# Kernel tuning notes

Hardware: AMD Instinct MI355X
Metric: run time of the kernel (lower is better)

## Reference

```python
import jax, jax.numpy as jnp
import numpy as np

B, S = 32768, 512  # rays, max bright spots (= 2*max_samples)


def setup_inputs() -> dict:
    key = jax.random.key(0)
    k1, k2, k3, k4, k5 = jax.random.split(key, 5)
    V = jax.random.normal(k1, (B, 3), dtype=jnp.float32)
    N = jax.random.normal(k2, (B, 3), dtype=jnp.float32)
    N = N / jnp.linalg.norm(N, axis=-1, keepdims=True)
    spots = jax.random.normal(k3, (S, 3), dtype=jnp.float32)
    spots = spots / jnp.linalg.norm(spots, axis=-1, keepdims=True)
    # prefix masks: num_ele[i] <= num_ray[i] <= S (matches kernel's start_ind-j indexing)
    num_ray = jax.random.randint(k4, (B,), S // 2, S + 1)
    num_ele = jax.random.randint(k5, (B,), 0, S // 2)
    j = jnp.arange(S)
    ray_mask = j[None, :] < num_ray[:, None]
    bright_mask = j[None, :] < num_ele[:, None]
    std = jnp.float32(0.05)  # pix_size
    return {"V": V, "N": N, "spots": spots, "ray_mask": ray_mask,
            "bright_mask": bright_mask, "std": std}


def reference(V, N, spots, ray_mask, bright_mask, std):
    Bn, Sn = bright_mask.shape
    # wp.randf(seed): uniform in [0,1), one per written component -> (B,S,3)
    u = jax.random.uniform(jax.random.key(42), (Bn, Sn, 3), dtype=spots.dtype)
    num_ele = bright_mask.sum(axis=1)            # n per row
    num_ray = ray_mask.sum(axis=1)               # start_ind = num_ray - 1
    j = jnp.arange(Sn)
    active = j[None, :] < num_ele[:, None]       # j in range(n)
    jit = spots[None, :, :] + std * u            # jittered light dirs (B,S,3)
    LdotN = jnp.einsum('bsd,bd->bs', jit, N)
    cond = active & (LdotN > 0.0)                # rejection test
    t = num_ray[:, None] - 1 - j[None, :]        # reversed write index
    t_safe = jnp.where(cond & (t >= 0) & (t < Sn), t, Sn)  # Sn -> dropped
    b_idx = jnp.arange(Bn)[:, None]
    Ls = jnp.zeros((Bn, Sn, 3), spots.dtype).at[b_idx, t_safe].set(jit, mode='drop')
    bmask = jnp.zeros((Bn, Sn), jnp.int32).at[b_idx, t_safe].set(1, mode='drop')
    return Ls, bmask.astype(bool)
```

## Files before the change

### kernel.cpp

```cpp
#include <hip/hip_runtime.h>


#define TF_ROUND(x0, x1, r) { x0 += x1; x1 = ((x1 << (r)) | (x1 >> (32 - (r)))); x1 ^= x0; }

__device__ __forceinline__ unsigned tf2x32_seed42_xor(unsigned x0, unsigned x1) {
  const unsigned k0 = 0u, k1 = 42u;
  const unsigned k2 = 0x1BD11BDAu ^ k0 ^ k1;
  x0 += k0; x1 += k1;
  TF_ROUND(x0,x1,13) TF_ROUND(x0,x1,15) TF_ROUND(x0,x1,26) TF_ROUND(x0,x1,6)
  x0 += k1; x1 += k2 + 1u;
  TF_ROUND(x0,x1,17) TF_ROUND(x0,x1,29) TF_ROUND(x0,x1,16) TF_ROUND(x0,x1,24)
  x0 += k2; x1 += k0 + 2u;
  TF_ROUND(x0,x1,13) TF_ROUND(x0,x1,15) TF_ROUND(x0,x1,26) TF_ROUND(x0,x1,6)
  x0 += k0; x1 += k1 + 3u;
  TF_ROUND(x0,x1,17) TF_ROUND(x0,x1,29) TF_ROUND(x0,x1,16) TF_ROUND(x0,x1,24)
  x0 += k1; x1 += k2 + 4u;
  TF_ROUND(x0,x1,13) TF_ROUND(x0,x1,15) TF_ROUND(x0,x1,26) TF_ROUND(x0,x1,6)
  x0 += k2; x1 += k0 + 5u;
  return x0 ^ x1;
}

typedef float f4v __attribute__((ext_vector_type(4)));

__device__ __forceinline__ int detect_mode(const unsigned char* m) {
  const unsigned char d0 = m[0], d1 = m[1], d4 = m[4];
  return (d0 == 0) ? 3 : ((d1 != 0) ? 0 : ((d4 != 0) ? 1 : 2));
}

__global__ __launch_bounds__(64, 8) void bis_row(
    const float* __restrict__ Nrm, const float* __restrict__ spots,
    const unsigned char* __restrict__ rmask, const unsigned char* __restrict__ emask,
    const float* __restrict__ stdp, float* __restrict__ Ls, float* __restrict__ bm)
{
  const int b = blockIdx.x;
  const int l = threadIdx.x;
  __shared__ f4v s_jit[256];

  const int mode = detect_mode(rmask);
  const unsigned base = (unsigned)b * 512u + (unsigned)(l << 3);

  int rcnt = 0, ecnt = 0;
  if (mode == 0) {
    const uint2 rv = *(const uint2*)(rmask + base);
    const uint2 ev = *(const uint2*)(emask + base);
    rcnt = __popc(rv.x & 0x01010101u) + __popc(rv.y & 0x01010101u);
    ecnt = __popc(ev.x & 0x01010101u) + __popc(ev.y & 0x01010101u);
  } else if (mode == 1) {
    const int* rp = (const int*)rmask + base; const int* ep = (const int*)emask + base;
    const int4 r0 = *(const int4*)rp, r1 = *(const int4*)(rp + 4);
    const int4 e0 = *(const int4*)ep, e1 = *(const int4*)(ep + 4);
    rcnt = (r0.x!=0)+(r0.y!=0)+(r0.z!=0)+(r0.w!=0)+(r1.x!=0)+(r1.y!=0)+(r1.z!=0)+(r1.w!=0);
    ecnt = (e0.x!=0)+(e0.y!=0)+(e0.z!=0)+(e0.w!=0)+(e1.x!=0)+(e1.y!=0)+(e1.z!=0)+(e1.w!=0);
  } else if (mode == 3) {
    const float* rp = (const float*)rmask + base; const float* ep = (const float*)emask + base;
    const float4 r0 = *(const float4*)rp, r1 = *(const float4*)(rp + 4);
    const float4 e0 = *(const float4*)ep, e1 = *(const float4*)(ep + 4);
    rcnt = (r0.x!=0.f)+(r0.y!=0.f)+(r0.z!=0.f)+(r0.w!=0.f)+(r1.x!=0.f)+(r1.y!=0.f)+(r1.z!=0.f)+(r1.w!=0.f);
    ecnt = (e0.x!=0.f)+(e0.y!=0.f)+(e0.z!=0.f)+(e0.w!=0.f)+(e1.x!=0.f)+(e1.y!=0.f)+(e1.z!=0.f)+(e1.w!=0.f);
  } else {
    const long long* rp = (const long long*)rmask; const long long* ep = (const long long*)emask;
    #pragma unroll
    for (int c = 0; c < 8; ++c) { rcnt += rp[base+c] != 0; ecnt += ep[base+c] != 0; }
  }
  unsigned pack = (unsigned)rcnt | ((unsigned)ecnt << 16);
  #pragma unroll
  for (int off = 1; off < 64; off <<= 1) pack += __shfl_xor(pack, off, 64);
  const int num_ray = (int)(pack & 0xFFFFu);
  const int num_ele = (int)(pack >> 16);

  if (num_ele > 0) {
    const float stdv = stdp[0];
    const float n0 = Nrm[b*3+0], n1 = Nrm[b*3+1], n2 = Nrm[b*3+2];
    for (int j = l; j < num_ele; j += 64) {
      const unsigned f = ((unsigned)b * 512u + (unsigned)j) * 3u;
      const float u0 = __uint_as_float((tf2x32_seed42_xor(0u, f + 0u) >> 9) | 0x3F800000u) - 1.0f;
      const float u1 = __uint_as_float((tf2x32_seed42_xor(0u, f + 1u) >> 9) | 0x3F800000u) - 1.0f;
      const float u2 = __uint_as_float((tf2x32_seed42_xor(0u, f + 2u) >> 9) | 0x3F800000u) - 1.0f;
      const float j0 = __fadd_rn(spots[j*3+0], __fmul_rn(stdv, u0));
      const float j1 = __fadd_rn(spots[j*3+1], __fmul_rn(stdv, u1));
      const float j2 = __fadd_rn(spots[j*3+2], __fmul_rn(stdv, u2));
      const float d  = __fadd_rn(__fadd_rn(__fmul_rn(j0,n0), __fmul_rn(j1,n1)),
                                 __fmul_rn(j2,n2));
      const bool acc = (d > 0.0f);
      f4v e; e.x = acc ? j0 : 0.f; e.y = acc ? j1 : 0.f; e.z = acc ? j2 : 0.f;
      e.w = acc ? 1.f : 0.f;
      s_jit[j] = e;
    }
  }
  __syncthreads();

  const int lo = num_ray - num_ele;
  const int hi = num_ray;
  const float* jrow = (const float*)s_jit;

  f4v* lsrow = (f4v*)(Ls + (size_t)b * 1536u);
  #pragma unroll
  for (int i = 0; i < 6; ++i) {
    const int g = i * 64 + l;
    const unsigned ff0 = (unsigned)(g << 2);
    const int s0 = (int)((ff0 * 43691u) >> 17);
    const int s1 = (int)(((ff0 + 3u) * 43691u) >> 17);
    f4v o = {0.f, 0.f, 0.f, 0.f};
    if (s1 >= lo && s0 < hi) {
      #pragma unroll
      for (int k = 0; k < 4; ++k) {
        const unsigned ff = ff0 + (unsigned)k;
        const unsigned s  = (ff * 43691u) >> 17;
        const unsigned comp = ff - 3u * s;
        const int jj = num_ray - 1 - (int)s;
        if (jj >= 0 && jj < num_ele) o[k] = jrow[(unsigned)jj * 4u + comp];
      }
    }
    lsrow[g] = o;
  }

  f4v* bmrow = (f4v*)(bm + (size_t)b * 512u);
  #pragma unroll
  for (int i = 0; i < 2; ++i) {
    const int g = i * 64 + l;
    const int sb = g << 2;
    f4v o = {0.f, 0.f, 0.f, 0.f};
    if (sb + 3 >= lo && sb < hi) {
      #pragma unroll
      for (int k = 0; k < 4; ++k) {
        const int jj = num_ray - 1 - (sb + k);
        if (jj >= 0 && jj < num_ele) o[k] = jrow[(unsigned)jj * 4u + 3u];
      }
    }
    bmrow[g] = o;
  }
}

struct F3 { float x, y, z; };

__global__ __launch_bounds__(512) void bis_kernel_s(
    const float* __restrict__ Nrm, const float* __restrict__ spots,
    const unsigned char* __restrict__ rmask, const unsigned char* __restrict__ emask,
    const float* __restrict__ stdp, float* __restrict__ Ls, float* __restrict__ bm,
    int S)
{
  const long long b = blockIdx.x;
  const int t = threadIdx.x;
  const int mode = detect_mode(rmask);

  const long long e = b * (long long)S + t;
  int rnz, enz;
  if (mode == 0)      { rnz = rmask[e] != 0;                     enz = emask[e] != 0; }
  else if (mode == 1) { rnz = ((const int*)rmask)[e] != 0;       enz = ((const int*)emask)[e] != 0; }
  else if (mode == 2) { rnz = ((const long long*)rmask)[e] != 0; enz = ((const long long*)emask)[e] != 0; }
  else                { rnz = ((const float*)rmask)[e] != 0.0f;  enz = ((const float*)emask)[e] != 0.0f; }

  __shared__ int s_nr[16], s_ne[16];
  const unsigned long long br = __ballot(rnz);
  const unsigned long long be = __ballot(enz);
  const int w = t >> 6;
  if ((t & 63) == 0) { s_nr[w] = __popcll(br); s_ne[w] = __popcll(be); }
  __syncthreads();
  const int nw = blockDim.x >> 6;
  int num_ray = 0, num_ele = 0;
  for (int i = 0; i < nw; ++i) { num_ray += s_nr[i]; num_ele += s_ne[i]; }

  const int j = num_ray - 1 - t;
  float o0 = 0.f, o1 = 0.f, o2 = 0.f, m = 0.f;
  if (j >= 0 && j < num_ele) {
    const float stdv = stdp[0];
    const float n0 = Nrm[b*3+0], n1 = Nrm[b*3+1], n2 = Nrm[b*3+2];
    const unsigned f = (unsigned)((b * (long long)S + j) * 3LL);
    const float u0 = __uint_as_float((tf2x32_seed42_xor(0u, f + 0u) >> 9) | 0x3F800000u) - 1.0f;
    const float u1 = __uint_as_float((tf2x32_seed42_xor(0u, f + 1u) >> 9) | 0x3F800000u) - 1.0f;
    const float u2 = __uint_as_float((tf2x32_seed42_xor(0u, f + 2u) >> 9) | 0x3F800000u) - 1.0f;
    const float j0 = __fadd_rn(spots[j*3+0], __fmul_rn(stdv, u0));
    const float j1 = __fadd_rn(spots[j*3+1], __fmul_rn(stdv, u1));
    const float j2 = __fadd_rn(spots[j*3+2], __fmul_rn(stdv, u2));
    const float d  = __fadd_rn(__fadd_rn(__fmul_rn(j0,n0), __fmul_rn(j1,n1)), __fmul_rn(j2,n2));
    if (d > 0.0f) { o0 = j0; o1 = j1; o2 = j2; m = 1.0f; }
  }

  const long long oidx = b * (long long)S + t;
  F3 v; v.x = o0; v.y = o1; v.z = o2;
  reinterpret_cast<F3*>(Ls)[oidx] = v;
  bm[oidx] = m;
}

extern "C" void kernel_launch(void* const* d_in, const int* in_sizes, int n_in,
                              void* d_out, int out_size, void* d_ws, size_t ws_size,
                              hipStream_t stream) {
  const float* Nrm = (const float*)d_in[1];
  const float* spots = (const float*)d_in[2];
  const unsigned char* rmask = (const unsigned char*)d_in[3];
  const unsigned char* emask = (const unsigned char*)d_in[4];
  const float* stdp = (const float*)d_in[5];

  const int B = in_sizes[0] / 3;
  const int S = in_sizes[2] / 3;

  float* out = (float*)d_out;
  float* Ls = out;
  float* bm = out + (long long)B * S * 3;

  if (S == 512) {
    dim3 grid((unsigned)B), block(64);
    hipLaunchKernelGGL(bis_row, grid, block, 0, stream,
                       Nrm, spots, rmask, emask, stdp, Ls, bm);
  } else {
    dim3 grid((unsigned)B), block((unsigned)S);
    hipLaunchKernelGGL(bis_kernel_s, grid, block, 0, stream,
                       Nrm, spots, rmask, emask, stdp, Ls, bm, S);
  }
}
```

Baseline: 82.88 us.

## Scatter jittered lights into output-layout LDS row and copy out as float4

```diff
diff --git a/kernel.cpp b/kernel.cpp
--- a/kernel.cpp
+++ b/kernel.cpp
@@ -27,14 +27,15 @@
   return (d0 == 0) ? 3 : ((d1 != 0) ? 0 : ((d4 != 0) ? 1 : 2));
 }
 
-__global__ __launch_bounds__(64, 8) void bis_row(
+__global__ __launch_bounds__(64, 8) void bis_direct3(
     const float* __restrict__ Nrm, const float* __restrict__ spots,
     const unsigned char* __restrict__ rmask, const unsigned char* __restrict__ emask,
     const float* __restrict__ stdp, float* __restrict__ Ls, float* __restrict__ bm)
 {
   const int b = blockIdx.x;
   const int l = threadIdx.x;
-  __shared__ f4v s_jit[256];
+  __shared__ f4v s_row[512];
+  float* rowf = (float*)s_row;
 
   const int mode = detect_mode(rmask);
   const unsigned base = (unsigned)b * 512u + (unsigned)(l << 3);
@@ -68,7 +69,17 @@
   const int num_ray = (int)(pack & 0xFFFFu);
   const int num_ele = (int)(pack >> 16);
 
-  if (num_ele > 0) {
+  const int lo = num_ray - num_ele;
+  const int hi = num_ray;
+  const bool nz = (num_ele > 0);
+
+  if (nz) {
+    const f4v z = {0.f, 0.f, 0.f, 0.f};
+    if (l == 0)      s_row[(3 * lo) >> 2] = z;
+    else if (l == 1) s_row[(3 * hi - 1) >> 2] = z;
+    else if (l == 2) s_row[384 + (lo >> 2)] = z;
+    else if (l == 3) s_row[384 + ((hi - 1) >> 2)] = z;
+
     const float stdv = stdp[0];
     const float n0 = Nrm[b*3+0], n1 = Nrm[b*3+1], n2 = Nrm[b*3+2];
     for (int j = l; j < num_ele; j += 64) {
@@ -82,51 +93,32 @@
       const float d  = __fadd_rn(__fadd_rn(__fmul_rn(j0,n0), __fmul_rn(j1,n1)),
                                  __fmul_rn(j2,n2));
       const bool acc = (d > 0.0f);
-      f4v e; e.x = acc ? j0 : 0.f; e.y = acc ? j1 : 0.f; e.z = acc ? j2 : 0.f;
-      e.w = acc ? 1.f : 0.f;
-      s_jit[j] = e;
+      const int t = num_ray - 1 - j;
+      rowf[3*t + 0] = acc ? j0 : 0.f;
+      rowf[3*t + 1] = acc ? j1 : 0.f;
+      rowf[3*t + 2] = acc ? j2 : 0.f;
+      rowf[1536 + t] = acc ? 1.0f : 0.f;
     }
   }
-  __syncthreads();
-
-  const int lo = num_ray - num_ele;
-  const int hi = num_ray;
-  const float* jrow = (const float*)s_jit;
-
+  asm volatile("s_waitcnt lgkmcnt(0)" ::: "memory");
+
+  const int flo = 3 * lo, fhi = 3 * hi;
   f4v* lsrow = (f4v*)(Ls + (size_t)b * 1536u);
   #pragma unroll
   for (int i = 0; i < 6; ++i) {
     const int g = i * 64 + l;
-    const unsigned ff0 = (unsigned)(g << 2);
-    const int s0 = (int)((ff0 * 43691u) >> 17);
-    const int s1 = (int)(((ff0 + 3u) * 43691u) >> 17);
+    const int f0 = g << 2;
     f4v o = {0.f, 0.f, 0.f, 0.f};
-    if (s1 >= lo && s0 < hi) {
-      #pragma unroll
-      for (int k = 0; k < 4; ++k) {
-        const unsigned ff = ff0 + (unsigned)k;
-        const unsigned s  = (ff * 43691u) >> 17;
-        const unsigned comp = ff - 3u * s;
-        const int jj = num_ray - 1 - (int)s;
-        if (jj >= 0 && jj < num_ele) o[k] = jrow[(unsigned)jj * 4u + comp];
-      }
-    }
+    if (nz && f0 + 3 >= flo && f0 < fhi) o = s_row[g];
     lsrow[g] = o;
   }
-
   f4v* bmrow = (f4v*)(bm + (size_t)b * 512u);
   #pragma unroll
   for (int i = 0; i < 2; ++i) {
     const int g = i * 64 + l;
-    const int sb = g << 2;
+    const int t0 = g << 2;
     f4v o = {0.f, 0.f, 0.f, 0.f};
-    if (sb + 3 >= lo && sb < hi) {
-      #pragma unroll
-      for (int k = 0; k < 4; ++k) {
-        const int jj = num_ray - 1 - (sb + k);
-        if (jj >= 0 && jj < num_ele) o[k] = jrow[(unsigned)jj * 4u + 3u];
-      }
-    }
+    if (nz && t0 + 3 >= lo && t0 < hi) o = s_row[384 + g];
     bmrow[g] = o;
   }
 }
@@ -200,7 +192,7 @@
 
   if (S == 512) {
     dim3 grid((unsigned)B), block(64);
-    hipLaunchKernelGGL(bis_row, grid, block, 0, stream,
+    hipLaunchKernelGGL(bis_direct3, grid, block, 0, stream,
                        Nrm, spots, rmask, emask, stdp, Ls, bm);
   } else {
     dim3 grid((unsigned)B), block((unsigned)S);
```

Result: faster. 79.92 us (median of 2 runs) (-3.6%).
